# Performance work log

Hardware: AMD Instinct MI355X
Metric: run time of the kernel (lower is better)

## Reference

```python
import jax, jax.numpy as jnp
import numpy as np

N_REUPLOADS = 3


def _qrun(x, Wp, bp, W1, b1, W2, b2):
    """Q-RUN layer: linear proj -> sin/cos reupload stack -> tiny per-channel MLP -> flatten.
    x: [..., in_dim]; Wp: [H2, in_dim]; W1: [mlp_h, 2*n_reuploads]; W2: [2, mlp_h].
    Returns [..., 2*H2].
    """
    p = jnp.einsum('...i,hi->...h', x, Wp) + bp                 # [..., H2]
    # features ordered [sin, cos, sin, cos, sin, cos] as in torch.stack of extend-ed list
    sc = jnp.stack([jnp.sin(p), jnp.cos(p)], axis=-1)           # [..., H2, 2]
    feats = jnp.tile(sc, (1,) * (sc.ndim - 1) + (N_REUPLOADS,))  # [..., H2, 6]
    h = jax.nn.relu(jnp.einsum('...k,mk->...m', feats, W1) + b1)  # [..., H2, 32]
    o = jnp.einsum('...m,om->...o', h, W2) + b2                 # [..., H2, 2]
    return o.reshape(o.shape[:-2] + (-1,))                      # flatten(start_dim=-2)


def setup_inputs() -> dict:
    key = jax.random.key(0)
    ks = jax.random.split(key, 20)
    H, I, MH, K = 5120, 27648, 32, 2 * N_REUPLOADS
    d = {}
    d['x'] = jax.random.normal(ks[0], (1, 256, H), dtype=jnp.float32)

    def mk(kbase, in_dim, out_half):
        k1, k2, k3, k4 = jax.random.split(kbase, 4)
        return (
            jax.random.normal(k1, (out_half, in_dim), jnp.float32) * (1.0 / np.sqrt(in_dim)),
            jnp.zeros((out_half,), jnp.float32),
            jax.random.normal(k2, (MH, K), jnp.float32) * 0.1,
            jnp.zeros((MH,), jnp.float32),
            jax.random.normal(k3, (2, MH), jnp.float32) * 0.01,
            jnp.zeros((2,), jnp.float32),
        )

    (d['Wg'], d['bg'], d['W1g'], d['b1g'], d['W2g'], d['b2g']) = mk(ks[1], H, I // 2)
    (d['Wu'], d['bu'], d['W1u'], d['b1u'], d['W2u'], d['b2u']) = mk(ks[2], H, I // 2)
    (d['Wd'], d['bd'], d['W1d'], d['b1d'], d['W2d'], d['b2d']) = mk(ks[3], I, H // 2)
    return d


def reference(x, Wg, bg, W1g, b1g, W2g, b2g,
              Wu, bu, W1u, b1u, W2u, b2u,
              Wd, bd, W1d, b1d, W2d, b2d):
    gate = _qrun(x, Wg, bg, W1g, b1g, W2g, b2g)   # [B,S,27648]
    up = _qrun(x, Wu, bu, W1u, b1u, W2u, b2u)     # [B,S,27648]
    h = jax.nn.silu(gate) * up
    return _qrun(h, Wd, bd, W1d, b1d, W2d, b2d)   # [B,S,5120]
```

## Files before the change

kernel.cpp:

```cpp
#include <hip/hip_runtime.h>
#include <stdint.h>

typedef unsigned short u16;
typedef __attribute__((ext_vector_type(8))) short short8;
typedef __attribute__((ext_vector_type(4))) float f32x4;

#define KGU  5120
#define NPD  2560
#define KD   27648
#define SPLITD 12
#define KCHD 2304
#define PEL (256*2560)

__device__ __forceinline__ uint32_t f2bf(float x) {
  uint32_t b = __float_as_uint(x);
  return (b + 0x7fffu + ((b >> 16) & 1u)) >> 16;
}
__device__ __forceinline__ uint32_t pk2(float lo, float hi) { return f2bf(lo) | (f2bf(hi) << 16); }
__device__ __forceinline__ uint32_t cvtpk(float lo, float hi) {
  uint32_t r;
  asm("v_cvt_pk_bf16_f32 %0, %1, %2" : "=v"(r) : "v"(lo), "v"(hi));
  return r;
}
__device__ __forceinline__ float silu(float x) {
  return x * __builtin_amdgcn_rcpf(1.f + __expf(-x));
}
#define MFMA16(a,b,c) __builtin_amdgcn_mfma_f32_16x16x32_bf16(a, b, c, 0, 0, 0)

__global__ __launch_bounds__(256) void k_cvt(const float* __restrict__ X, u16* __restrict__ XF) {
  const int kt = blockIdx.x;
  const int lane = threadIdx.x & 63, wv = threadIdx.x >> 6;
#pragma unroll
  for (int ii = 0; ii < 4; ++ii) {
    const int mt = wv * 4 + ii;
    const float* src = X + (size_t)(mt * 16 + (lane & 15)) * KGU + kt * 32 + (lane >> 4) * 8;
    float4 f0 = *(const float4*)src;
    float4 f1 = *(const float4*)(src + 4);
    uint4 v;
    v.x = cvtpk(f0.x, f0.y); v.y = cvtpk(f0.z, f0.w);
    v.z = cvtpk(f1.x, f1.y); v.w = cvtpk(f1.z, f1.w);
    *(uint4*)(XF + ((size_t)(kt * 16 + mt) * 64 + lane) * 8) = v;
  }
}

__global__ __launch_bounds__(512, 4)
void k_gu(const u16* __restrict__ XF,
          const float* __restrict__ Wg, const float* __restrict__ bg,
          const float* __restrict__ W1g, const float* __restrict__ b1g,
          const float* __restrict__ W2g, const float* __restrict__ b2g,
          const float* __restrict__ Wu, const float* __restrict__ bu,
          const float* __restrict__ W1u, const float* __restrict__ b1u,
          const float* __restrict__ W2u, const float* __restrict__ b2u,
          u16* __restrict__ HF) {
  __shared__ __align__(16) char smem[16384 + 1536];
  const int tid = threadIdx.x, lane = tid & 63, wid = tid >> 6;
  const int wm = wid >> 1, wn = wid & 1;
  const int s_ = lane & 15, quad = lane >> 4;
  const int bx = blockIdx.x;
  const int w = (bx & 7) * 54 + (bx >> 3);
  const int j0p = w * 32;

  float4* mc4 = (float4*)(smem + 16384);
  float*  mc1 = (float*)(smem + 16384 + 1024);
  if (tid < 64) {
    int sel = tid >> 5, m = tid & 31;
    const float* w1 = (sel ? W1u : W1g) + m * 6;
    const float* b1 = sel ? b1u : b1g;
    const float* w2 = sel ? W2u : W2g;
    mc4[sel * 32 + m] = make_float4(w1[0] + w1[2] + w1[4], w1[1] + w1[3] + w1[5], b1[m], w2[m]);
    mc1[sel * 32 + m] = w2[32 + m];
  }

  const int r_loc = 8 * wid + (lane >> 3);
  const float* srcB = ((r_loc & 1) ? Wu : Wg) + (size_t)(j0p + (r_loc >> 1)) * KGU + (lane & 7) * 8;
  const int bwr = r_loc * 128 + (((lane & 7) ^ (r_loc & 7)) << 4);
  const int rb = wn * 32 + s_;
  const int rsw = s_ & 7;

  const short8* XFp = (const short8*)XF;
  const short8* paB = XFp + ((size_t)wm * 4) * 64 + lane;

  f32x4 acc[4][2];
#pragma unroll
  for (int i = 0; i < 4; ++i) { acc[i][0] = (f32x4)0.f; acc[i][1] = (f32x4)0.f; }
  float4 sr[4][2];
  short8 Ag[2][4];

#pragma unroll
  for (int j = 0; j < 4; ++j) {
    sr[j][0] = *(const float4*)(srcB + j * 64);
    sr[j][1] = *(const float4*)(srcB + j * 64 + 4);
  }
#pragma unroll
  for (int kk = 0; kk < 2; ++kk)
#pragma unroll
    for (int mi = 0; mi < 4; ++mi) Ag[kk][mi] = paB[(size_t)kk * 1024 + mi * 64];
  {
    uint4 v;
    v.x = cvtpk(sr[0][0].x, sr[0][0].y); v.y = cvtpk(sr[0][0].z, sr[0][0].w);
    v.z = cvtpk(sr[0][1].x, sr[0][1].y); v.w = cvtpk(sr[0][1].z, sr[0][1].w);
    *(uint4*)(smem + bwr) = v;
  }
  asm volatile("s_waitcnt lgkmcnt(0)" ::: "memory");
  __builtin_amdgcn_sched_barrier(0);
  __builtin_amdgcn_s_barrier();

#pragma unroll 1
  for (int tb = 0; tb < 20; ++tb) {
#pragma unroll
    for (int j = 0; j < 4; ++j) {
      const int st = tb * 4 + j;
      const char* buf = smem + (j & 1) * 8192;
#pragma unroll
      for (int kk = 0; kk < 2; ++kk) {
        const int so = ((kk * 4 + quad) ^ rsw) << 4;
        short8 b0 = *(const short8*)(buf + rb * 128 + so);
        short8 b1 = *(const short8*)(buf + (rb + 16) * 128 + so);
        __builtin_amdgcn_s_setprio(1);
        acc[0][0] = MFMA16(Ag[kk][0], b0, acc[0][0]); acc[0][1] = MFMA16(Ag[kk][0], b1, acc[0][1]);
        acc[1][0] = MFMA16(Ag[kk][1], b0, acc[1][0]); acc[1][1] = MFMA16(Ag[kk][1], b1, acc[1][1]);
        acc[2][0] = MFMA16(Ag[kk][2], b0, acc[2][0]); acc[2][1] = MFMA16(Ag[kk][2], b1, acc[2][1]);
        acc[3][0] = MFMA16(Ag[kk][3], b0, acc[3][0]); acc[3][1] = MFMA16(Ag[kk][3], b1, acc[3][1]);
        __builtin_amdgcn_s_setprio(0);
        const int stn = (st < 79) ? st + 1 : 79;
        const short8* pa = paB + (size_t)(stn * 2 + kk) * 1024;
#pragma unroll
        for (int mi = 0; mi < 4; ++mi) Ag[kk][mi] = pa[mi * 64];
      }
      const int jn = (j + 1) & 3;
      char* bufn = smem + (((j & 1) ^ 1)) * 8192;
      uint4 v;
      v.x = cvtpk(sr[jn][0].x, sr[jn][0].y); v.y = cvtpk(sr[jn][0].z, sr[jn][0].w);
      v.z = cvtpk(sr[jn][1].x, sr[jn][1].y); v.w = cvtpk(sr[jn][1].z, sr[jn][1].w);
      *(uint4*)(bufn + bwr) = v;
      const int stf = (st + 5 < 80) ? st + 5 : 79;
      sr[jn][0] = *(const float4*)(srcB + stf * 64);
      sr[jn][1] = *(const float4*)(srcB + stf * 64 + 4);
      asm volatile("s_waitcnt lgkmcnt(0)" ::: "memory");
      __builtin_amdgcn_sched_barrier(0);
      __builtin_amdgcn_s_barrier();
    }
  }

  const int sel = lane & 1;
  const float b2v0 = sel ? b2u[0] : b2g[0];
  const float b2v1 = sel ? b2u[1] : b2g[1];
  const float4* mcs = mc4 + sel * 32;
  const float*  mcw = mc1 + sel * 32;
  char* HFb = (char*)HF;
#pragma unroll
  for (int ni = 0; ni < 2; ++ni) {
    const int c = wn * 32 + ni * 16 + s_;
    const int j = j0p + (c >> 1);
    const float bp = sel ? bu[j] : bg[j];
#pragma unroll
    for (int mi = 0; mi < 4; ++mi) {
      float sv[4], cv[4], o0[4], o1[4];
#pragma unroll
      for (int e = 0; e < 4; ++e) {
        float p = acc[mi][ni][e] + bp;
        sv[e] = __sinf(p); cv[e] = __cosf(p);
        o0[e] = b2v0; o1[e] = b2v1;
      }
#pragma unroll 4
      for (int m = 0; m < 32; ++m) {
        float4 k4 = mcs[m]; float w2b = mcw[m];
#pragma unroll
        for (int e = 0; e < 4; ++e) {
          float hh = fmaxf(fmaf(sv[e], k4.x, fmaf(cv[e], k4.y, k4.z)), 0.f);
          o0[e] = fmaf(hh, k4.w, o0[e]);
          o1[e] = fmaf(hh, w2b, o1[e]);
        }
      }
#pragma unroll
      for (int e = 0; e < 4; ++e) {
        float t0 = __shfl_xor(o0[e], 1);
        float t1 = __shfl_xor(o1[e], 1);
        float g0 = sel ? t0 : o0[e];
        float u0 = sel ? o0[e] : t0;
        float g1 = sel ? t1 : o1[e];
        float u1 = sel ? o1[e] : t1;
        float h0 = silu(g0) * u0, h1 = silu(g1) * u1;
        if (!sel) {
          const int row = wm * 64 + mi * 16 + quad * 4 + e;
          const int kt2 = j >> 4, mt2 = wm * 4 + mi;
          const int lf2 = (row & 15) + 16 * ((j >> 2) & 3);
          *(uint32_t*)(HFb + (size_t)(kt2 * 16 + mt2) * 1024 + lf2 * 16 + (j & 3) * 4)
              = pk2(h0, h1);
        }
      }
    }
  }
}

__global__ __launch_bounds__(512, 4)
void k_down(const u16* __restrict__ HF, const float* __restrict__ Wd, float* __restrict__ P2) {
  __shared__ __align__(16) char smem[16384];
  const int tid = threadIdx.x, lane = tid & 63, wid = tid >> 6;
  const int wm = wid >> 1, wn = wid & 1;
  const int s_ = lane & 15, quad = lane >> 4;
  const int bx = blockIdx.x;
  const int w = (bx & 7) * 60 + (bx >> 3);
  const int sk = w / 40, nt = w - sk * 40;
  const int n0 = nt * 64;

  const int r_loc = 8 * wid + (lane >> 3);
  const float* srcB = Wd + (size_t)(n0 + r_loc) * KD + sk * KCHD + (lane & 7) * 8;
  const int bwr = r_loc * 128 + (((lane & 7) ^ (r_loc & 7)) << 4);
  const int rb = wn * 32 + s_;
  const int rsw = s_ & 7;

  const short8* HFp = (const short8*)HF;
  const short8* paB = HFp + ((size_t)(sk * 72) * 16 + wm * 4) * 64 + lane;

  f32x4 acc[4][2];
#pragma unroll
  for (int i = 0; i < 4; ++i) { acc[i][0] = (f32x4)0.f; acc[i][1] = (f32x4)0.f; }
  float4 sr[4][2];
  short8 Ag[2][4];

#pragma unroll
  for (int j = 0; j < 4; ++j) {
    sr[j][0] = *(const float4*)(srcB + j * 64);
    sr[j][1] = *(const float4*)(srcB + j * 64 + 4);
  }
#pragma unroll
  for (int kk = 0; kk < 2; ++kk)
#pragma unroll
    for (int mi = 0; mi < 4; ++mi) Ag[kk][mi] = paB[(size_t)kk * 1024 + mi * 64];
  {
    uint4 v;
    v.x = cvtpk(sr[0][0].x, sr[0][0].y); v.y = cvtpk(sr[0][0].z, sr[0][0].w);
    v.z = cvtpk(sr[0][1].x, sr[0][1].y); v.w = cvtpk(sr[0][1].z, sr[0][1].w);
    *(uint4*)(smem + bwr) = v;
  }
  asm volatile("s_waitcnt lgkmcnt(0)" ::: "memory");
  __builtin_amdgcn_sched_barrier(0);
  __builtin_amdgcn_s_barrier();

#pragma unroll 1
  for (int tb = 0; tb < 9; ++tb) {
#pragma unroll
    for (int j = 0; j < 4; ++j) {
      const int st = tb * 4 + j;
      const char* buf = smem + (j & 1) * 8192;
#pragma unroll
      for (int kk = 0; kk < 2; ++kk) {
        const int so = ((kk * 4 + quad) ^ rsw) << 4;
        short8 b0 = *(const short8*)(buf + rb * 128 + so);
        short8 b1 = *(const short8*)(buf + (rb + 16) * 128 + so);
        __builtin_amdgcn_s_setprio(1);
        acc[0][0] = MFMA16(Ag[kk][0], b0, acc[0][0]); acc[0][1] = MFMA16(Ag[kk][0], b1, acc[0][1]);
        acc[1][0] = MFMA16(Ag[kk][1], b0, acc[1][0]); acc[1][1] = MFMA16(Ag[kk][1], b1, acc[1][1]);
        acc[2][0] = MFMA16(Ag[kk][2], b0, acc[2][0]); acc[2][1] = MFMA16(Ag[kk][2], b1, acc[2][1]);
        acc[3][0] = MFMA16(Ag[kk][3], b0, acc[3][0]); acc[3][1] = MFMA16(Ag[kk][3], b1, acc[3][1]);
        __builtin_amdgcn_s_setprio(0);
        const int stn = (st < 35) ? st + 1 : 35;
        const short8* pa = paB + (size_t)(stn * 2 + kk) * 1024;
#pragma unroll
        for (int mi = 0; mi < 4; ++mi) Ag[kk][mi] = pa[mi * 64];
      }
      const int jn = (j + 1) & 3;
      char* bufn = smem + (((j & 1) ^ 1)) * 8192;
      uint4 v;
      v.x = cvtpk(sr[jn][0].x, sr[jn][0].y); v.y = cvtpk(sr[jn][0].z, sr[jn][0].w);
      v.z = cvtpk(sr[jn][1].x, sr[jn][1].y); v.w = cvtpk(sr[jn][1].z, sr[jn][1].w);
      *(uint4*)(bufn + bwr) = v;
      const int stf = (st + 5 < 36) ? st + 5 : 35;
      sr[jn][0] = *(const float4*)(srcB + stf * 64);
      sr[jn][1] = *(const float4*)(srcB + stf * 64 + 4);
      asm volatile("s_waitcnt lgkmcnt(0)" ::: "memory");
      __builtin_amdgcn_sched_barrier(0);
      __builtin_amdgcn_s_barrier();
    }
  }

  float* P = P2 + (size_t)sk * PEL;
#pragma unroll
  for (int mi = 0; mi < 4; ++mi) {
    int mrow = wm * 64 + mi * 16 + (quad << 2);
#pragma unroll
    for (int ni = 0; ni < 2; ++ni) {
      int n = n0 + wn * 32 + ni * 16 + s_;
#pragma unroll
      for (int e = 0; e < 4; ++e)
        P[(size_t)(mrow + e) * NPD + n] = acc[mi][ni][e];
    }
  }
}

__global__ __launch_bounds__(256) void k_fin(const float* __restrict__ P2, const float* __restrict__ bd,
    const float* __restrict__ W1d, const float* __restrict__ b1d, const float* __restrict__ W2d,
    const float* __restrict__ b2d, float* __restrict__ out) {
  __shared__ float4 mc0[32];
  __shared__ float mc1[32];
  const int tid = threadIdx.x;
  if (tid < 32) {
    const float* w = W1d + tid * 6;
    mc0[tid] = make_float4(w[0] + w[2] + w[4], w[1] + w[3] + w[5], b1d[tid], W2d[tid]);
    mc1[tid] = W2d[32 + tid];
  }
  __syncthreads();
  const int idx = blockIdx.x * 256 + tid;
  const int m = idx / NPD, j = idx - m * NPD;
  float p = bd[j];
#pragma unroll
  for (int sk = 0; sk < SPLITD; ++sk) p += P2[(size_t)sk * PEL + idx];
  float s = __sinf(p), c = __cosf(p);
  float o0 = b2d[0], o1 = b2d[1];
#pragma unroll 4
  for (int mm = 0; mm < 32; ++mm) {
    float4 k = mc0[mm];
    float hh = fmaxf(fmaf(s, k.x, fmaf(c, k.y, k.z)), 0.f);
    o0 = fmaf(hh, k.w, o0);
    o1 = fmaf(hh, mc1[mm], o1);
  }
  *(float2*)&out[(size_t)m * 5120 + 2 * j] = make_float2(o0, o1);
}

extern "C" void kernel_launch(void* const* d_in, const int* in_sizes, int n_in,
                              void* d_out, int out_size, void* d_ws, size_t ws_size,
                              hipStream_t stream) {
  const float* x   = (const float*)d_in[0];
  const float* Wg  = (const float*)d_in[1];
  const float* bg  = (const float*)d_in[2];
  const float* W1g = (const float*)d_in[3];
  const float* b1g = (const float*)d_in[4];
  const float* W2g = (const float*)d_in[5];
  const float* b2g = (const float*)d_in[6];
  const float* Wu  = (const float*)d_in[7];
  const float* bu  = (const float*)d_in[8];
  const float* W1u = (const float*)d_in[9];
  const float* b1u = (const float*)d_in[10];
  const float* W2u = (const float*)d_in[11];
  const float* b2u = (const float*)d_in[12];
  const float* Wd  = (const float*)d_in[13];
  const float* bd  = (const float*)d_in[14];
  const float* W1d = (const float*)d_in[15];
  const float* b1d = (const float*)d_in[16];
  const float* W2d = (const float*)d_in[17];
  const float* b2d = (const float*)d_in[18];
  char* ws = (char*)d_ws;
  u16*  XF = (u16*)ws;
  u16*  HF = (u16*)(ws + 2621440);
  float* P2 = (float*)(ws + 16777216);
  if (ws_size < 48234496u) return;

  k_cvt<<<dim3(160), dim3(256), 0, stream>>>(x, XF);
  k_gu<<<dim3(432), dim3(512), 0, stream>>>(XF, Wg, bg, W1g, b1g, W2g, b2g,
                                            Wu, bu, W1u, b1u, W2u, b2u, HF);
  k_down<<<dim3(480), dim3(512), 0, stream>>>(HF, Wd, P2);
  k_fin<<<dim3(2560), dim3(256), 0, stream>>>(P2, bd, W1d, b1d, W2d, b2d, (float*)d_out);
}
```

Baseline: 315.8 us.

## Use 16-wave blocks with one M-tile per wave and larger K stages

Both GEMM kernels move from 512-thread blocks, where each wave computes a 4x2 grid of 16x16 tiles, to 1024-thread blocks where each of 16 waves owns one 16-row M tile across all 64 N columns. Each stage now loads a 128-wide K slab of weights (32 KB double-buffered LDS), so there are half as many barriers per K. The goal is fewer registers per wave and more waves in flight to hide the fp32 weight-streaming latency. The cost is that each wave reads four B fragments from LDS per A fragment, where before it was two per four, which raises LDS traffic per MFMA. A 1024-thread block with a 16-wave barrier also brings more synchronisation overhead.

```diff
diff --git a/kernel.cpp b/kernel.cpp
--- a/kernel.cpp
+++ b/kernel.cpp
@@ -43,7 +43,7 @@
   }
 }
 
-__global__ __launch_bounds__(512, 4)
+__global__ __launch_bounds__(1024, 6)
 void k_gu(const u16* __restrict__ XF,
           const float* __restrict__ Wg, const float* __restrict__ bg,
           const float* __restrict__ W1g, const float* __restrict__ b1g,
@@ -52,16 +52,15 @@
           const float* __restrict__ W1u, const float* __restrict__ b1u,
           const float* __restrict__ W2u, const float* __restrict__ b2u,
           u16* __restrict__ HF) {
-  __shared__ __align__(16) char smem[16384 + 1536];
+  __shared__ __align__(16) char smem[32768 + 1536];
   const int tid = threadIdx.x, lane = tid & 63, wid = tid >> 6;
-  const int wm = wid >> 1, wn = wid & 1;
   const int s_ = lane & 15, quad = lane >> 4;
   const int bx = blockIdx.x;
   const int w = (bx & 7) * 54 + (bx >> 3);
   const int j0p = w * 32;
 
-  float4* mc4 = (float4*)(smem + 16384);
-  float*  mc1 = (float*)(smem + 16384 + 1024);
+  float4* mc4 = (float4*)(smem + 32768);
+  float*  mc1 = (float*)(smem + 32768 + 1024);
   if (tid < 64) {
     int sel = tid >> 5, m = tid & 31;
     const float* w1 = (sel ? W1u : W1g) + m * 6;
@@ -71,75 +70,73 @@
     mc1[sel * 32 + m] = w2[32 + m];
   }
 
-  const int r_loc = 8 * wid + (lane >> 3);
-  const float* srcB = ((r_loc & 1) ? Wu : Wg) + (size_t)(j0p + (r_loc >> 1)) * KGU + (lane & 7) * 8;
-  const int bwr = r_loc * 128 + (((lane & 7) ^ (r_loc & 7)) << 4);
-  const int rb = wn * 32 + s_;
-  const int rsw = s_ & 7;
-
-  const short8* XFp = (const short8*)XF;
-  const short8* paB = XFp + ((size_t)wm * 4) * 64 + lane;
-
-  f32x4 acc[4][2];
-#pragma unroll
-  for (int i = 0; i < 4; ++i) { acc[i][0] = (f32x4)0.f; acc[i][1] = (f32x4)0.f; }
-  float4 sr[4][2];
-  short8 Ag[2][4];
-
-#pragma unroll
-  for (int j = 0; j < 4; ++j) {
-    sr[j][0] = *(const float4*)(srcB + j * 64);
-    sr[j][1] = *(const float4*)(srcB + j * 64 + 4);
-  }
-#pragma unroll
-  for (int kk = 0; kk < 2; ++kk)
-#pragma unroll
-    for (int mi = 0; mi < 4; ++mi) Ag[kk][mi] = paB[(size_t)kk * 1024 + mi * 64];
+  const int brow = tid >> 4, bk8 = tid & 15;
+  const float* srcB = ((brow & 1) ? Wu : Wg) + (size_t)(j0p + (brow >> 1)) * KGU + bk8 * 8;
+  const int bwr = ((tid >> 3) & 1) * 8192 + brow * 128 + (((tid & 7) ^ (brow & 7)) << 4);
+
+  const short8* paB = (const short8*)XF + (size_t)wid * 64 + lane;
+
+  f32x4 acc[4];
+#pragma unroll
+  for (int i = 0; i < 4; ++i) acc[i] = (f32x4)0.f;
+  short8 A0, A1;
+  float4 sA0, sA1, sB0, sB1;
+
+  sA0 = *(const float4*)(srcB);       sA1 = *(const float4*)(srcB + 4);
+  sB0 = *(const float4*)(srcB + 128); sB1 = *(const float4*)(srcB + 132);
+  A0 = paB[0]; A1 = paB[1024];
   {
     uint4 v;
-    v.x = cvtpk(sr[0][0].x, sr[0][0].y); v.y = cvtpk(sr[0][0].z, sr[0][0].w);
-    v.z = cvtpk(sr[0][1].x, sr[0][1].y); v.w = cvtpk(sr[0][1].z, sr[0][1].w);
+    v.x = cvtpk(sA0.x, sA0.y); v.y = cvtpk(sA0.z, sA0.w);
+    v.z = cvtpk(sA1.x, sA1.y); v.w = cvtpk(sA1.z, sA1.w);
     *(uint4*)(smem + bwr) = v;
   }
+  sA0 = *(const float4*)(srcB + 256); sA1 = *(const float4*)(srcB + 260);
   asm volatile("s_waitcnt lgkmcnt(0)" ::: "memory");
   __builtin_amdgcn_sched_barrier(0);
   __builtin_amdgcn_s_barrier();
 
-#pragma unroll 1
-  for (int tb = 0; tb < 20; ++tb) {
-#pragma unroll
-    for (int j = 0; j < 4; ++j) {
-      const int st = tb * 4 + j;
-      const char* buf = smem + (j & 1) * 8192;
-#pragma unroll
-      for (int kk = 0; kk < 2; ++kk) {
-        const int so = ((kk * 4 + quad) ^ rsw) << 4;
-        short8 b0 = *(const short8*)(buf + rb * 128 + so);
-        short8 b1 = *(const short8*)(buf + (rb + 16) * 128 + so);
-        __builtin_amdgcn_s_setprio(1);
-        acc[0][0] = MFMA16(Ag[kk][0], b0, acc[0][0]); acc[0][1] = MFMA16(Ag[kk][0], b1, acc[0][1]);
-        acc[1][0] = MFMA16(Ag[kk][1], b0, acc[1][0]); acc[1][1] = MFMA16(Ag[kk][1], b1, acc[1][1]);
-        acc[2][0] = MFMA16(Ag[kk][2], b0, acc[2][0]); acc[2][1] = MFMA16(Ag[kk][2], b1, acc[2][1]);
-        acc[3][0] = MFMA16(Ag[kk][3], b0, acc[3][0]); acc[3][1] = MFMA16(Ag[kk][3], b1, acc[3][1]);
-        __builtin_amdgcn_s_setprio(0);
-        const int stn = (st < 79) ? st + 1 : 79;
-        const short8* pa = paB + (size_t)(stn * 2 + kk) * 1024;
-#pragma unroll
-        for (int mi = 0; mi < 4; ++mi) Ag[kk][mi] = pa[mi * 64];
-      }
-      const int jn = (j + 1) & 3;
-      char* bufn = smem + (((j & 1) ^ 1)) * 8192;
+  auto kkstep = [&](const char* bb, int gbase, short8& Au, int ktn) {
+    const int g = ((gbase + quad) ^ (s_ & 7)) << 4;
+    const char* p = bb + s_ * 128 + g;
+    short8 b0 = *(const short8*)(p);
+    short8 b1 = *(const short8*)(p + 2048);
+    short8 b2 = *(const short8*)(p + 4096);
+    short8 b3 = *(const short8*)(p + 6144);
+    __builtin_amdgcn_s_setprio(1);
+    acc[0] = MFMA16(Au, b0, acc[0]);
+    acc[1] = MFMA16(Au, b1, acc[1]);
+    acc[2] = MFMA16(Au, b2, acc[2]);
+    acc[3] = MFMA16(Au, b3, acc[3]);
+    __builtin_amdgcn_s_setprio(0);
+    Au = paB[(size_t)ktn * 1024];
+  };
+  auto period = [&](int st, float4& W0, float4& W1) {
+    const char* buf = smem + (st & 1) * 16384;
+    const int base = st * 4;
+    kkstep(buf,        0, A0, (base + 2 > 159) ? 159 : base + 2);
+    kkstep(buf,        4, A1, (base + 3 > 159) ? 159 : base + 3);
+    kkstep(buf + 8192, 0, A0, (base + 4 > 159) ? 159 : base + 4);
+    kkstep(buf + 8192, 4, A1, (base + 5 > 159) ? 159 : base + 5);
+    if (st < 39) {
+      char* bufn = smem + ((st + 1) & 1) * 16384;
       uint4 v;
-      v.x = cvtpk(sr[jn][0].x, sr[jn][0].y); v.y = cvtpk(sr[jn][0].z, sr[jn][0].w);
-      v.z = cvtpk(sr[jn][1].x, sr[jn][1].y); v.w = cvtpk(sr[jn][1].z, sr[jn][1].w);
+      v.x = cvtpk(W0.x, W0.y); v.y = cvtpk(W0.z, W0.w);
+      v.z = cvtpk(W1.x, W1.y); v.w = cvtpk(W1.z, W1.w);
       *(uint4*)(bufn + bwr) = v;
-      const int stf = (st + 5 < 80) ? st + 5 : 79;
-      sr[jn][0] = *(const float4*)(srcB + stf * 64);
-      sr[jn][1] = *(const float4*)(srcB + stf * 64 + 4);
+      const int stf = (st + 3 > 39) ? 39 : st + 3;
+      W0 = *(const float4*)(srcB + stf * 128);
+      W1 = *(const float4*)(srcB + stf * 128 + 4);
       asm volatile("s_waitcnt lgkmcnt(0)" ::: "memory");
       __builtin_amdgcn_sched_barrier(0);
       __builtin_amdgcn_s_barrier();
     }
+  };
+
+#pragma unroll 1
+  for (int sp = 0; sp < 20; ++sp) {
+    period(2 * sp,     sB0, sB1);
+    period(2 * sp + 1, sA0, sA1);
   }
 
   const int sel = lane & 1;
@@ -149,143 +146,133 @@
   const float*  mcw = mc1 + sel * 32;
   char* HFb = (char*)HF;
 #pragma unroll
-  for (int ni = 0; ni < 2; ++ni) {
-    const int c = wn * 32 + ni * 16 + s_;
+  for (int ni = 0; ni < 4; ++ni) {
+    const int c = ni * 16 + s_;
     const int j = j0p + (c >> 1);
     const float bp = sel ? bu[j] : bg[j];
-#pragma unroll
-    for (int mi = 0; mi < 4; ++mi) {
-      float sv[4], cv[4], o0[4], o1[4];
+    float sv[4], cv[4], o0[4], o1[4];
+#pragma unroll
+    for (int e = 0; e < 4; ++e) {
+      float p = acc[ni][e] + bp;
+      sv[e] = __sinf(p); cv[e] = __cosf(p);
+      o0[e] = b2v0; o1[e] = b2v1;
+    }
+#pragma unroll 4
+    for (int m = 0; m < 32; ++m) {
+      float4 k4 = mcs[m]; float w2b = mcw[m];
 #pragma unroll
       for (int e = 0; e < 4; ++e) {
-        float p = acc[mi][ni][e] + bp;
-        sv[e] = __sinf(p); cv[e] = __cosf(p);
-        o0[e] = b2v0; o1[e] = b2v1;
+        float hh = fmaxf(fmaf(sv[e], k4.x, fmaf(cv[e], k4.y, k4.z)), 0.f);
+        o0[e] = fmaf(hh, k4.w, o0[e]);
+        o1[e] = fmaf(hh, w2b, o1[e]);
       }
-#pragma unroll 4
-      for (int m = 0; m < 32; ++m) {
-        float4 k4 = mcs[m]; float w2b = mcw[m];
-#pragma unroll
-        for (int e = 0; e < 4; ++e) {
-          float hh = fmaxf(fmaf(sv[e], k4.x, fmaf(cv[e], k4.y, k4.z)), 0.f);
-          o0[e] = fmaf(hh, k4.w, o0[e]);
-          o1[e] = fmaf(hh, w2b, o1[e]);
-        }
+    }
+#pragma unroll
+    for (int e = 0; e < 4; ++e) {
+      float t0 = __shfl_xor(o0[e], 1);
+      float t1 = __shfl_xor(o1[e], 1);
+      float g0 = sel ? t0 : o0[e];
+      float u0 = sel ? o0[e] : t0;
+      float g1 = sel ? t1 : o1[e];
+      float u1 = sel ? o1[e] : t1;
+      float h0 = silu(g0) * u0, h1 = silu(g1) * u1;
+      if (!sel) {
+        const int row = wid * 16 + quad * 4 + e;
+        const int kt2 = j >> 4;
+        const int lf2 = (row & 15) + 16 * ((j >> 2) & 3);
+        *(uint32_t*)(HFb + ((size_t)(kt2 * 16 + wid) * 64 + lf2) * 16 + (j & 3) * 4)
+            = pk2(h0, h1);
       }
-#pragma unroll
-      for (int e = 0; e < 4; ++e) {
-        float t0 = __shfl_xor(o0[e], 1);
-        float t1 = __shfl_xor(o1[e], 1);
-        float g0 = sel ? t0 : o0[e];
-        float u0 = sel ? o0[e] : t0;
-        float g1 = sel ? t1 : o1[e];
-        float u1 = sel ? o1[e] : t1;
-        float h0 = silu(g0) * u0, h1 = silu(g1) * u1;
-        if (!sel) {
-          const int row = wm * 64 + mi * 16 + quad * 4 + e;
-          const int kt2 = j >> 4, mt2 = wm * 4 + mi;
-          const int lf2 = (row & 15) + 16 * ((j >> 2) & 3);
-          *(uint32_t*)(HFb + (size_t)(kt2 * 16 + mt2) * 1024 + lf2 * 16 + (j & 3) * 4)
-              = pk2(h0, h1);
-        }
-      }
-    }
-  }
-}
-
-__global__ __launch_bounds__(512, 4)
+    }
+  }
+}
+
+__global__ __launch_bounds__(1024, 6)
 void k_down(const u16* __restrict__ HF, const float* __restrict__ Wd, float* __restrict__ P2) {
-  __shared__ __align__(16) char smem[16384];
+  __shared__ __align__(16) char smem[32768];
   const int tid = threadIdx.x, lane = tid & 63, wid = tid >> 6;
-  const int wm = wid >> 1, wn = wid & 1;
   const int s_ = lane & 15, quad = lane >> 4;
   const int bx = blockIdx.x;
   const int w = (bx & 7) * 60 + (bx >> 3);
   const int sk = w / 40, nt = w - sk * 40;
   const int n0 = nt * 64;
 
-  const int r_loc = 8 * wid + (lane >> 3);
-  const float* srcB = Wd + (size_t)(n0 + r_loc) * KD + sk * KCHD + (lane & 7) * 8;
-  const int bwr = r_loc * 128 + (((lane & 7) ^ (r_loc & 7)) << 4);
-  const int rb = wn * 32 + s_;
-  const int rsw = s_ & 7;
-
-  const short8* HFp = (const short8*)HF;
-  const short8* paB = HFp + ((size_t)(sk * 72) * 16 + wm * 4) * 64 + lane;
-
-  f32x4 acc[4][2];
-#pragma unroll
-  for (int i = 0; i < 4; ++i) { acc[i][0] = (f32x4)0.f; acc[i][1] = (f32x4)0.f; }
-  float4 sr[4][2];
-  short8 Ag[2][4];
-
-#pragma unroll
-  for (int j = 0; j < 4; ++j) {
-    sr[j][0] = *(const float4*)(srcB + j * 64);
-    sr[j][1] = *(const float4*)(srcB + j * 64 + 4);
-  }
-#pragma unroll
-  for (int kk = 0; kk < 2; ++kk)
-#pragma unroll
-    for (int mi = 0; mi < 4; ++mi) Ag[kk][mi] = paB[(size_t)kk * 1024 + mi * 64];
+  const int brow = tid >> 4, bk8 = tid & 15;
+  const float* srcB = Wd + (size_t)(n0 + brow) * KD + sk * KCHD + bk8 * 8;
+  const int bwr = ((tid >> 3) & 1) * 8192 + brow * 128 + (((tid & 7) ^ (brow & 7)) << 4);
+
+  const short8* paB = (const short8*)HF + ((size_t)(sk * 72) * 16 + wid) * 64 + lane;
+
+  f32x4 acc[4];
+#pragma unroll
+  for (int i = 0; i < 4; ++i) acc[i] = (f32x4)0.f;
+  short8 A0, A1;
+  float4 sA0, sA1, sB0, sB1;
+
+  sA0 = *(const float4*)(srcB);       sA1 = *(const float4*)(srcB + 4);
+  sB0 = *(const float4*)(srcB + 128); sB1 = *(const float4*)(srcB + 132);
+  A0 = paB[0]; A1 = paB[1024];
   {
     uint4 v;
-    v.x = cvtpk(sr[0][0].x, sr[0][0].y); v.y = cvtpk(sr[0][0].z, sr[0][0].w);
-    v.z = cvtpk(sr[0][1].x, sr[0][1].y); v.w = cvtpk(sr[0][1].z, sr[0][1].w);
+    v.x = cvtpk(sA0.x, sA0.y); v.y = cvtpk(sA0.z, sA0.w);
+    v.z = cvtpk(sA1.x, sA1.y); v.w = cvtpk(sA1.z, sA1.w);
     *(uint4*)(smem + bwr) = v;
   }
+  sA0 = *(const float4*)(srcB + 256); sA1 = *(const float4*)(srcB + 260);
   asm volatile("s_waitcnt lgkmcnt(0)" ::: "memory");
   __builtin_amdgcn_sched_barrier(0);
   __builtin_amdgcn_s_barrier();
 
-#pragma unroll 1
-  for (int tb = 0; tb < 9; ++tb) {
-#pragma unroll
-    for (int j = 0; j < 4; ++j) {
-      const int st = tb * 4 + j;
-      const char* buf = smem + (j & 1) * 8192;
-#pragma unroll
-      for (int kk = 0; kk < 2; ++kk) {
-        const int so = ((kk * 4 + quad) ^ rsw) << 4;
-        short8 b0 = *(const short8*)(buf + rb * 128 + so);
-        short8 b1 = *(const short8*)(buf + (rb + 16) * 128 + so);
-        __builtin_amdgcn_s_setprio(1);
-        acc[0][0] = MFMA16(Ag[kk][0], b0, acc[0][0]); acc[0][1] = MFMA16(Ag[kk][0], b1, acc[0][1]);
-        acc[1][0] = MFMA16(Ag[kk][1], b0, acc[1][0]); acc[1][1] = MFMA16(Ag[kk][1], b1, acc[1][1]);
-        acc[2][0] = MFMA16(Ag[kk][2], b0, acc[2][0]); acc[2][1] = MFMA16(Ag[kk][2], b1, acc[2][1]);
-        acc[3][0] = MFMA16(Ag[kk][3], b0, acc[3][0]); acc[3][1] = MFMA16(Ag[kk][3], b1, acc[3][1]);
-        __builtin_amdgcn_s_setprio(0);
-        const int stn = (st < 35) ? st + 1 : 35;
-        const short8* pa = paB + (size_t)(stn * 2 + kk) * 1024;
-#pragma unroll
-        for (int mi = 0; mi < 4; ++mi) Ag[kk][mi] = pa[mi * 64];
-      }
-      const int jn = (j + 1) & 3;
-      char* bufn = smem + (((j & 1) ^ 1)) * 8192;
+  auto kkstep = [&](const char* bb, int gbase, short8& Au, int ktn) {
+    const int g = ((gbase + quad) ^ (s_ & 7)) << 4;
+    const char* p = bb + s_ * 128 + g;
+    short8 b0 = *(const short8*)(p);
+    short8 b1 = *(const short8*)(p + 2048);
+    short8 b2 = *(const short8*)(p + 4096);
+    short8 b3 = *(const short8*)(p + 6144);
+    __builtin_amdgcn_s_setprio(1);
+    acc[0] = MFMA16(Au, b0, acc[0]);
+    acc[1] = MFMA16(Au, b1, acc[1]);
+    acc[2] = MFMA16(Au, b2, acc[2]);
+    acc[3] = MFMA16(Au, b3, acc[3]);
+    __builtin_amdgcn_s_setprio(0);
+    Au = paB[(size_t)ktn * 1024];
+  };
+  auto period = [&](int st, float4& W0, float4& W1) {
+    const char* buf = smem + (st & 1) * 16384;
+    const int base = st * 4;
+    kkstep(buf,        0, A0, (base + 2 > 71) ? 71 : base + 2);
+    kkstep(buf,        4, A1, (base + 3 > 71) ? 71 : base + 3);
+    kkstep(buf + 8192, 0, A0, (base + 4 > 71) ? 71 : base + 4);
+    kkstep(buf + 8192, 4, A1, (base + 5 > 71) ? 71 : base + 5);
+    if (st < 17) {
+      char* bufn = smem + ((st + 1) & 1) * 16384;
       uint4 v;
-      v.x = cvtpk(sr[jn][0].x, sr[jn][0].y); v.y = cvtpk(sr[jn][0].z, sr[jn][0].w);
-      v.z = cvtpk(sr[jn][1].x, sr[jn][1].y); v.w = cvtpk(sr[jn][1].z, sr[jn][1].w);
+      v.x = cvtpk(W0.x, W0.y); v.y = cvtpk(W0.z, W0.w);
+      v.z = cvtpk(W1.x, W1.y); v.w = cvtpk(W1.z, W1.w);
       *(uint4*)(bufn + bwr) = v;
-      const int stf = (st + 5 < 36) ? st + 5 : 35;
-      sr[jn][0] = *(const float4*)(srcB + stf * 64);
-      sr[jn][1] = *(const float4*)(srcB + stf * 64 + 4);
+      const int stf = (st + 3 > 17) ? 17 : st + 3;
+      W0 = *(const float4*)(srcB + stf * 128);
+      W1 = *(const float4*)(srcB + stf * 128 + 4);
       asm volatile("s_waitcnt lgkmcnt(0)" ::: "memory");
       __builtin_amdgcn_sched_barrier(0);
       __builtin_amdgcn_s_barrier();
     }
+  };
+
+#pragma unroll 1
+  for (int sp = 0; sp < 9; ++sp) {
+    period(2 * sp,     sB0, sB1);
+    period(2 * sp + 1, sA0, sA1);
   }
 
   float* P = P2 + (size_t)sk * PEL;
 #pragma unroll
-  for (int mi = 0; mi < 4; ++mi) {
-    int mrow = wm * 64 + mi * 16 + (quad << 2);
-#pragma unroll
-    for (int ni = 0; ni < 2; ++ni) {
-      int n = n0 + wn * 32 + ni * 16 + s_;
-#pragma unroll
-      for (int e = 0; e < 4; ++e)
-        P[(size_t)(mrow + e) * NPD + n] = acc[mi][ni][e];
-    }
+  for (int ni = 0; ni < 4; ++ni) {
+    const int n = n0 + ni * 16 + s_;
+#pragma unroll
+    for (int e = 0; e < 4; ++e)
+      P[(size_t)(wid * 16 + quad * 4 + e) * NPD + n] = acc[ni][e];
   }
 }
 
@@ -347,8 +334,8 @@
   if (ws_size < 48234496u) return;
 
   k_cvt<<<dim3(160), dim3(256), 0, stream>>>(x, XF);
-  k_gu<<<dim3(432), dim3(512), 0, stream>>>(XF, Wg, bg, W1g, b1g, W2g, b2g,
-                                            Wu, bu, W1u, b1u, W2u, b2u, HF);
-  k_down<<<dim3(480), dim3(512), 0, stream>>>(HF, Wd, P2);
+  k_gu<<<dim3(432), dim3(1024), 0, stream>>>(XF, Wg, bg, W1g, b1g, W2g, b2g,
+                                             Wu, bu, W1u, b1u, W2u, b2u, HF);
+  k_down<<<dim3(480), dim3(1024), 0, stream>>>(HF, Wd, P2);
   k_fin<<<dim3(2560), dim3(256), 0, stream>>>(P2, bd, W1d, b1d, W2d, b2d, (float*)d_out);
 }
```

Result: no change. 315.9 us (+0.0%).
